# Optimization experiments

Hardware: AMD Instinct MI355X
Metric: run time of the kernel (lower is better)

Reference implementation:

```python
import jax, jax.numpy as jnp
import numpy as np

N, TI, ENC_DIM, DEC_DIM, ATT_DIM = 32, 2000, 512, 512, 512


def setup_inputs() -> dict:
    key = jax.random.key(0)
    ks = jax.random.split(key, 8)
    enc_pad = jax.random.normal(ks[0], (N, TI, ENC_DIM), dtype=jnp.float32)
    dec_prev = jax.random.normal(ks[1], (N, DEC_DIM), dtype=jnp.float32)
    ali_prev = jax.random.uniform(ks[2], (N, TI), dtype=jnp.float32)
    # lengths in [Ti//2, Ti], force one full-length row (module uses max(enc_len) as mask width)
    enc_len = jax.random.randint(ks[3], (N,), TI // 2, TI + 1)
    enc_len = enc_len.at[0].set(TI)
    # learned params (nn.Linear layout: W [out, in])
    s_e = 1.0 / np.sqrt(ENC_DIM)
    s_d = 1.0 / np.sqrt(DEC_DIM)
    s_a = 1.0 / np.sqrt(ATT_DIM)
    W_enc = jax.random.uniform(ks[4], (ATT_DIM, ENC_DIM), minval=-s_e, maxval=s_e, dtype=jnp.float32)
    b_enc = jax.random.uniform(ks[5], (ATT_DIM,), minval=-s_e, maxval=s_e, dtype=jnp.float32)
    W_dec = jax.random.uniform(ks[6], (ATT_DIM, DEC_DIM), minval=-s_d, maxval=s_d, dtype=jnp.float32)
    w_v = jax.random.uniform(ks[7], (ATT_DIM,), minval=-s_a, maxval=s_a, dtype=jnp.float32)
    return {"enc_pad": enc_pad, "enc_len": enc_len, "dec_prev": dec_prev,
            "ali_prev": ali_prev, "W_enc": W_enc, "b_enc": b_enc,
            "W_dec": W_dec, "w_v": w_v}


def reference(enc_pad, enc_len, dec_prev, ali_prev, W_enc, b_enc, W_dec, w_v):
    # enc_part: N x Ti x A  (enc_proj with bias)
    enc_part = jnp.einsum('ntd,ad->nta', enc_pad, W_enc) + b_enc
    # dec_part: N x A  (dec_proj, no bias)
    dec_part = jnp.einsum('nd,ad->na', dec_prev, W_dec)
    # additive score e = w^T tanh(enc_part + dec_part): N x Ti
    e = jnp.einsum('nta,a->nt', jnp.tanh(enc_part + dec_part[:, None, :]), w_v)
    # padding mask: positions >= enc_len are masked
    mask = jnp.arange(e.shape[1]) >= enc_len[:, None]  # N x Ti
    e = jnp.where(mask, -jnp.inf, e)
    ali = jax.nn.softmax(e, axis=1)  # N x Ti
    ctx = jnp.einsum('nt,ntd->nd', ali, enc_pad)  # N x D_enc
    return (ali, ctx)
```

## Files before the change

### kernel.cpp

```cpp
#include <hip/hip_runtime.h>
#include <stdint.h>


#define NB  32
#define TI  2000
#define ED  512
#define AD  512
#define M_TOT (NB * TI)
#define NSPLIT 20
#define TCHUNK (TI / NSPLIT)
#define MT  500
#define MT2 250
#define KT  8
#define TILE_BYTES  16384
#define TILE_HALVES 8192

using f16x8 = __attribute__((ext_vector_type(8))) _Float16;
using f32x4 = __attribute__((ext_vector_type(4))) float;

__device__ __forceinline__ int swz(int r, int c) { return (r * 128 + c) ^ ((r & 7) << 4); }

#define GLD16(g, l)                                                     \
    __builtin_amdgcn_global_load_lds(                                   \
        (const __attribute__((address_space(1))) void*)(g),             \
        (__attribute__((address_space(3))) void*)(l), 16, 0, 0)

__device__ __forceinline__ float fast_tanh(float s) {
    s = fminf(fmaxf(s, -15.f), 15.f);
    float t = __expf(2.f * s);
    return __fdividef(t - 1.f, t + 1.f);
}

__global__ void k_convert(const float* __restrict__ enc, const float* __restrict__ Wenc,
                          _Float16* __restrict__ X16, _Float16* __restrict__ W16,
                          const float* __restrict__ dec_prev, const float* __restrict__ W_dec,
                          const float* __restrict__ b_enc, float* __restrict__ db) {
    __shared__ float xd[ED];
    int bx = blockIdx.x;
    int tid = threadIdx.x;
    if (bx >= MT * KT + 32) {
        int n = bx - (MT * KT + 32);
        for (int k = tid; k < ED; k += 256) xd[k] = dec_prev[n * ED + k];
        __syncthreads();
        for (int a = tid; a < AD; a += 256) {
            const float* wr = W_dec + (size_t)a * ED;
            float s = 0.f;
#pragma unroll 8
            for (int k = 0; k < ED; k += 4) {
                float4 w = *(const float4*)(wr + k);
                s += xd[k] * w.x + xd[k + 1] * w.y + xd[k + 2] * w.z + xd[k + 3] * w.w;
            }
            db[n * AD + a] = s + b_enc[a];
        }
        return;
    }
    const float* src;
    char* dstb;
    if (bx < MT * KT) {
        int mt = bx >> 3, kt = bx & 7;
        src  = enc + (size_t)mt * 128 * ED + kt * 64;
        dstb = (char*)(X16 + (size_t)bx * TILE_HALVES);
    } else {
        int wt = bx - MT * KT;
        int at = wt >> 3, kt = wt & 7;
        src  = Wenc + (size_t)at * 128 * ED + kt * 64;
        dstb = (char*)(W16 + (size_t)wt * TILE_HALVES);
    }
#pragma unroll
    for (int i = 0; i < 4; ++i) {
        int o  = i * 4096 + tid * 16;
        int r  = o >> 7;
        int c2 = o & 127;
        const float* s = src + (size_t)r * ED + (c2 >> 1);
        float4 a = *(const float4*)s;
        float4 b = *(const float4*)(s + 4);
        f16x8 h;
        h[0] = (_Float16)a.x; h[1] = (_Float16)a.y; h[2] = (_Float16)a.z; h[3] = (_Float16)a.w;
        h[4] = (_Float16)b.x; h[5] = (_Float16)b.y; h[6] = (_Float16)b.z; h[7] = (_Float16)b.w;
        *(f16x8*)(dstb + swz(r, c2)) = h;
    }
}

__global__ void k_decdb(const float* __restrict__ dec_prev,
                        const float* __restrict__ W_dec,
                        const float* __restrict__ b_enc,
                        float* __restrict__ db) {
    int n = blockIdx.x;
    __shared__ float xd[ED];
    for (int k = threadIdx.x; k < ED; k += 256) xd[k] = dec_prev[n * ED + k];
    __syncthreads();
    for (int a = threadIdx.x; a < AD; a += 256) {
        const float* wr = W_dec + (size_t)a * ED;
        float s = 0.f;
#pragma unroll 8
        for (int k = 0; k < ED; k += 4) {
            float4 w = *(const float4*)(wr + k);
            s += xd[k] * w.x + xd[k + 1] * w.y + xd[k + 2] * w.z + xd[k + 3] * w.w;
        }
        db[n * AD + a] = s + b_enc[a];
    }
}

__device__ __forceinline__ void stage_tiles(const char* xb, const char* wb,
                                            char* dA, char* dB, int kt, int o) {
    const char* xs = xb + kt * TILE_BYTES + o;
    const char* ws = wb + kt * TILE_BYTES + o;
    GLD16(xs,                           dA + o);
    GLD16(xs + 8192,                    dA + o + 8192);
    GLD16(xs + KT * TILE_BYTES,         dA + o + 16384);
    GLD16(xs + KT * TILE_BYTES + 8192,  dA + o + 24576);
    GLD16(ws,                           dB + o);
    GLD16(ws + 8192,                    dB + o + 8192);
    GLD16(ws + KT * TILE_BYTES,         dB + o + 16384);
    GLD16(ws + KT * TILE_BYTES + 8192,  dB + o + 24576);
}

__launch_bounds__(512, 2)
__global__ void k_score256(const _Float16* __restrict__ X16, const _Float16* __restrict__ W16,
                           const float* __restrict__ db, const float* __restrict__ wv,
                           float* __restrict__ e_part) {
    __shared__ alignas(16) char As0[32768];
    __shared__ alignas(16) char As1[32768];
    __shared__ alignas(16) char Bs0[32768];
    __shared__ alignas(16) char Bs1[32768];

    int fid = blockIdx.x;
    int g = fid >> 4, r = fid & 15;
    int at2 = r >> 3;
    int mt2 = g * 8 + (r & 7);
    if (mt2 >= MT2) return;

    const int tid  = threadIdx.x;
    const int lane = tid & 63;
    const int w    = tid >> 6;
    const int wm   = w >> 2;
    const int wn   = w & 3;
    const int m0   = mt2 * 256;
    const int a0   = at2 * 256;

    const char* xb = (const char*)X16 + (size_t)(mt2 * 2 * KT) * TILE_BYTES;
    const char* wb = (const char*)W16 + (size_t)(at2 * 2 * KT) * TILE_BYTES;

    const int lr    = lane & 15;
    const int lk2   = (lane >> 4) * 16;
    const int wmoff = wm * 16384;
    const int wnoff = (wn >> 1) * 16384;
    const int wnrow = (wn & 1) * 64;
    const int o     = tid * 16;

    f32x4 acc[8][4];
#pragma unroll
    for (int rb = 0; rb < 8; ++rb)
#pragma unroll
        for (int cb = 0; cb < 4; ++cb) acc[rb][cb] = (f32x4){0.f, 0.f, 0.f, 0.f};

#define COMPUTE(sA, sB)                                                          \
    {                                                                            \
        _Pragma("unroll")                                                        \
        for (int kb = 0; kb < 2; ++kb) {                                         \
            f16x8 aF[8], bF[4];                                                  \
            _Pragma("unroll")                                                    \
            for (int rb = 0; rb < 8; ++rb)                                       \
                aF[rb] = *(const f16x8*)((sA) + wmoff + swz(rb * 16 + lr, kb * 64 + lk2)); \
            _Pragma("unroll")                                                    \
            for (int cb = 0; cb < 4; ++cb)                                       \
                bF[cb] = *(const f16x8*)((sB) + wnoff + swz(wnrow + cb * 16 + lr, kb * 64 + lk2)); \
            __builtin_amdgcn_s_setprio(1);                                       \
            _Pragma("unroll")                                                    \
            for (int rb = 0; rb < 8; ++rb)                                       \
                _Pragma("unroll")                                                \
                for (int cb = 0; cb < 4; ++cb)                                   \
                    acc[rb][cb] = __builtin_amdgcn_mfma_f32_16x16x32_f16(        \
                        aF[rb], bF[cb], acc[rb][cb], 0, 0, 0);                   \
            __builtin_amdgcn_s_setprio(0);                                       \
        }                                                                        \
    }

    stage_tiles(xb, wb, As0, Bs0, 0, o); __syncthreads();
    stage_tiles(xb, wb, As1, Bs1, 1, o); COMPUTE(As0, Bs0); __syncthreads();
    stage_tiles(xb, wb, As0, Bs0, 2, o); COMPUTE(As1, Bs1); __syncthreads();
    stage_tiles(xb, wb, As1, Bs1, 3, o); COMPUTE(As0, Bs0); __syncthreads();
    stage_tiles(xb, wb, As0, Bs0, 4, o); COMPUTE(As1, Bs1); __syncthreads();
    stage_tiles(xb, wb, As1, Bs1, 5, o); COMPUTE(As0, Bs0); __syncthreads();
    stage_tiles(xb, wb, As0, Bs0, 6, o); COMPUTE(As1, Bs1); __syncthreads();
    stage_tiles(xb, wb, As1, Bs1, 7, o); COMPUTE(As0, Bs0); __syncthreads();
    COMPUTE(As1, Bs1); __syncthreads();
#undef COMPUTE

    float* e_red = (float*)As0;
    const int lg = lane >> 4;
    float wvv[4];
#pragma unroll
    for (int cb = 0; cb < 4; ++cb) wvv[cb] = wv[a0 + wn * 64 + cb * 16 + lr];

#pragma unroll
    for (int rb = 0; rb < 8; ++rb) {
#pragma unroll
        for (int i = 0; i < 4; ++i) {
            int row_local = wm * 128 + rb * 16 + lg * 4 + i;
            int m = m0 + row_local;
            int n = m / TI;
            const float* dbp = db + (size_t)n * AD + a0 + wn * 64;
            float rs = 0.f;
#pragma unroll
            for (int cb = 0; cb < 4; ++cb) {
                float s = acc[rb][cb][i] + dbp[cb * 16 + lr];
                rs += fast_tanh(s) * wvv[cb];
            }
            rs += __shfl_xor(rs, 1);
            rs += __shfl_xor(rs, 2);
            rs += __shfl_xor(rs, 4);
            rs += __shfl_xor(rs, 8);
            if (lr == 0) e_red[wn * 256 + row_local] = rs;
        }
    }
    __syncthreads();
    if (tid < 256)
        e_part[(size_t)at2 * M_TOT + m0 + tid] =
            e_red[tid] + e_red[256 + tid] + e_red[512 + tid] + e_red[768 + tid];
}

__launch_bounds__(256, 2)
__global__ void k_score_fb(const float* __restrict__ X, const float* __restrict__ W,
                           const float* __restrict__ db, const float* __restrict__ wv,
                           float* __restrict__ e_part) {
    __shared__ alignas(16) _Float16 Xs[128][72];
    __shared__ alignas(16) _Float16 Ws[128][72];
    __shared__ float e_red[2][128];

    const int tid = threadIdx.x, lane = tid & 63, wid = tid >> 6;
    const int wr = wid >> 1, wc = wid & 1;
    const int m0 = blockIdx.x * 128, a0 = blockIdx.y * 128;

    f32x4 acc[4][4];
#pragma unroll
    for (int rb = 0; rb < 4; ++rb)
#pragma unroll
        for (int cb = 0; cb < 4; ++cb) acc[rb][cb] = (f32x4){0.f, 0.f, 0.f, 0.f};

    const int lr = lane & 15;
    const int lk = (lane >> 4) << 3;

    for (int kt = 0; kt < ED; kt += 64) {
#pragma unroll
        for (int i = 0; i < 4; ++i) {
            int idx = tid + i * 256, r = idx >> 3, c = (idx & 7) << 3;
            const float* gx = X + (size_t)(m0 + r) * ED + kt + c;
            float4 x0 = *(const float4*)gx, x1 = *(const float4*)(gx + 4);
            f16x8 hx;
            hx[0] = (_Float16)x0.x; hx[1] = (_Float16)x0.y; hx[2] = (_Float16)x0.z; hx[3] = (_Float16)x0.w;
            hx[4] = (_Float16)x1.x; hx[5] = (_Float16)x1.y; hx[6] = (_Float16)x1.z; hx[7] = (_Float16)x1.w;
            *(f16x8*)&Xs[r][c] = hx;
            const float* gw = W + (size_t)(a0 + r) * ED + kt + c;
            float4 w0 = *(const float4*)gw, w1 = *(const float4*)(gw + 4);
            f16x8 hw;
            hw[0] = (_Float16)w0.x; hw[1] = (_Float16)w0.y; hw[2] = (_Float16)w0.z; hw[3] = (_Float16)w0.w;
            hw[4] = (_Float16)w1.x; hw[5] = (_Float16)w1.y; hw[6] = (_Float16)w1.z; hw[7] = (_Float16)w1.w;
            *(f16x8*)&Ws[r][c] = hw;
        }
        __syncthreads();
#pragma unroll
        for (int kb = 0; kb < 64; kb += 32) {
            f16x8 aF[4], bF[4];
#pragma unroll
            for (int rb = 0; rb < 4; ++rb) aF[rb] = *(const f16x8*)&Xs[wr * 64 + rb * 16 + lr][kb + lk];
#pragma unroll
            for (int cb = 0; cb < 4; ++cb) bF[cb] = *(const f16x8*)&Ws[wc * 64 + cb * 16 + lr][kb + lk];
#pragma unroll
            for (int rb = 0; rb < 4; ++rb)
#pragma unroll
                for (int cb = 0; cb < 4; ++cb)
                    acc[rb][cb] = __builtin_amdgcn_mfma_f32_16x16x32_f16(aF[rb], bF[cb], acc[rb][cb], 0, 0, 0);
        }
        __syncthreads();
    }

    const int lg = lane >> 4;
    float wvv[4];
#pragma unroll
    for (int cb = 0; cb < 4; ++cb) wvv[cb] = wv[a0 + wc * 64 + cb * 16 + lr];
#pragma unroll
    for (int rb = 0; rb < 4; ++rb) {
#pragma unroll
        for (int i = 0; i < 4; ++i) {
            int row_local = wr * 64 + rb * 16 + lg * 4 + i;
            int m = m0 + row_local;
            int n = m / TI;
            const float* dbp = db + (size_t)n * AD + a0 + wc * 64;
            float rs = 0.f;
#pragma unroll
            for (int cb = 0; cb < 4; ++cb) {
                float s = acc[rb][cb][i] + dbp[cb * 16 + lr];
                rs += fast_tanh(s) * wvv[cb];
            }
            rs += __shfl_xor(rs, 1);
            rs += __shfl_xor(rs, 2);
            rs += __shfl_xor(rs, 4);
            rs += __shfl_xor(rs, 8);
            if (lr == 0) e_red[wc][row_local] = rs;
        }
    }
    __syncthreads();
    if (tid < 128)
        e_part[(size_t)blockIdx.y * M_TOT + m0 + tid] = e_red[0][tid] + e_red[1][tid];
}

__global__ void k_softmax(const float* __restrict__ e_part,
                          const int* __restrict__ enc_len,
                          float* __restrict__ ali, int nparts) {
    int n = blockIdx.x;
    int len = enc_len[n];
    __shared__ float se[TI];
    __shared__ float redm[4];
    __shared__ float reds[4];
    int tid = threadIdx.x;
    int lane = tid & 63, wid = tid >> 6;

    for (int t = tid; t < TI; t += 256) {
        float s = 0.f;
        for (int p = 0; p < nparts; ++p) s += e_part[(size_t)p * M_TOT + n * TI + t];
        se[t] = s;
    }
    __syncthreads();

    float mx = -1e30f;
    for (int t = tid; t < len; t += 256) mx = fmaxf(mx, se[t]);
#pragma unroll
    for (int o = 32; o >= 1; o >>= 1) mx = fmaxf(mx, __shfl_xor(mx, o));
    if (lane == 0) redm[wid] = mx;
    __syncthreads();
    mx = fmaxf(fmaxf(redm[0], redm[1]), fmaxf(redm[2], redm[3]));

    float sm = 0.f;
    for (int t = tid; t < len; t += 256) {
        float ex = __expf(se[t] - mx);
        se[t] = ex;
        sm += ex;
    }
#pragma unroll
    for (int o = 32; o >= 1; o >>= 1) sm += __shfl_xor(sm, o);
    if (lane == 0) reds[wid] = sm;
    __syncthreads();
    float inv = 1.f / (reds[0] + reds[1] + reds[2] + reds[3]);

    for (int t = tid; t < TI; t += 256)
        ali[n * TI + t] = (t < len) ? se[t] * inv : 0.f;
}

__global__ void k_ctxpart16(const _Float16* __restrict__ X16, const float* __restrict__ ali,
                            float* __restrict__ cpart) {
    int s = blockIdx.x, n = blockIdx.y;
    int tid = threadIdx.x;
    int sub = tid >> 6;
    int dc  = (tid & 63) * 8;
    int ktile = dc >> 6;
    int c2 = (dc & 63) * 2;
    float acc[8] = {0.f, 0.f, 0.f, 0.f, 0.f, 0.f, 0.f, 0.f};
    for (int t = s * TCHUNK + sub; t < (s + 1) * TCHUNK; t += 4) {
        int m = n * TI + t;
        int mt2 = m >> 7, r = m & 127;
        const char* p = (const char*)(X16 + (size_t)(mt2 * KT + ktile) * TILE_HALVES);
        f16x8 v = *(const f16x8*)(p + swz(r, c2));
        float a = ali[m];
#pragma unroll
        for (int j = 0; j < 8; ++j) acc[j] = fmaf(a, (float)v[j], acc[j]);
    }
    __shared__ float red[4][ED];
#pragma unroll
    for (int j = 0; j < 8; ++j) red[sub][dc + j] = acc[j];
    __syncthreads();
    if (sub == 0) {
#pragma unroll
        for (int j = 0; j < 8; ++j) {
            float sm = red[0][dc + j] + red[1][dc + j] + red[2][dc + j] + red[3][dc + j];
            cpart[((size_t)(n * NSPLIT + s)) * ED + dc + j] = sm;
        }
    }
}

__global__ void k_ctxpart(const float* __restrict__ enc,
                          const float* __restrict__ ali,
                          float* __restrict__ cpart) {
    int s = blockIdx.x;
    int n = blockIdx.y;
    int d0 = threadIdx.x * 2;
    const float* base = enc + ((size_t)n * TI + s * TCHUNK) * ED + d0;
    const float* ap = ali + n * TI + s * TCHUNK;
    float ax = 0.f, ay = 0.f;
#pragma unroll 4
    for (int t = 0; t < TCHUNK; ++t) {
        float a = ap[t];
        float2 v = *(const float2*)(base + (size_t)t * ED);
        ax = fmaf(a, v.x, ax);
        ay = fmaf(a, v.y, ay);
    }
    float2 r; r.x = ax; r.y = ay;
    *(float2*)&cpart[((size_t)(n * NSPLIT + s)) * ED + d0] = r;
}

__global__ void k_ctxred(const float* __restrict__ cpart, float* __restrict__ ctx) {
    int n = blockIdx.x;
    for (int d = threadIdx.x; d < ED; d += 256) {
        float sum = 0.f;
#pragma unroll
        for (int s = 0; s < NSPLIT; ++s) sum += cpart[((size_t)(n * NSPLIT + s)) * ED + d];
        ctx[(size_t)n * ED + d] = sum;
    }
}

extern "C" void kernel_launch(void* const* d_in, const int* in_sizes, int n_in,
                              void* d_out, int out_size, void* d_ws, size_t ws_size,
                              hipStream_t stream) {
    const float* enc_pad  = (const float*)d_in[0];
    const int*   enc_len  = (const int*)d_in[1];
    const float* dec_prev = (const float*)d_in[2];
    const float* W_enc    = (const float*)d_in[4];
    const float* b_enc    = (const float*)d_in[5];
    const float* W_dec    = (const float*)d_in[6];
    const float* w_v      = (const float*)d_in[7];

    float* out = (float*)d_out;
    float* ali = out;
    float* ctx = out + M_TOT;

    float* ws     = (float*)d_ws;
    float* db     = ws;
    float* e_part = ws + NB * AD;
    float* cpart  = e_part + 4 * M_TOT;
    size_t fp_floats = (size_t)NB * AD + 4 * M_TOT + (size_t)NB * NSPLIT * ED;
    _Float16* X16 = (_Float16*)((char*)d_ws + fp_floats * 4);
    _Float16* W16 = X16 + (size_t)MT * KT * TILE_HALVES;
    size_t need = fp_floats * 4 + ((size_t)MT * KT + 32) * TILE_BYTES;
    bool big = ws_size >= need;

    if (big) {
        hipLaunchKernelGGL(k_convert, dim3(MT * KT + 64), dim3(256), 0, stream,
                           enc_pad, W_enc, X16, W16, dec_prev, W_dec, b_enc, db);
        hipLaunchKernelGGL(k_score256, dim3(512), dim3(512), 0, stream,
                           X16, W16, db, w_v, e_part);
        hipLaunchKernelGGL(k_softmax, dim3(NB), dim3(256), 0, stream, e_part, enc_len, ali, 2);
        hipLaunchKernelGGL(k_ctxpart16, dim3(NSPLIT, NB), dim3(256), 0, stream, X16, ali, cpart);
    } else {
        hipLaunchKernelGGL(k_decdb, dim3(NB), dim3(256), 0, stream, dec_prev, W_dec, b_enc, db);
        hipLaunchKernelGGL(k_score_fb, dim3(MT, 4), dim3(256), 0, stream,
                           enc_pad, W_enc, db, w_v, e_part);
        hipLaunchKernelGGL(k_softmax, dim3(NB), dim3(256), 0, stream, e_part, enc_len, ali, 4);
        hipLaunchKernelGGL(k_ctxpart, dim3(NSPLIT, NB), dim3(256), 0, stream, enc_pad, ali, cpart);
    }
    hipLaunchKernelGGL(k_ctxred, dim3(NB), dim3(256), 0, stream, cpart, ctx);
}
```

Before: 138.9 us.

## Convert encoder fp32 to fp16 inside score GEMM instead of a separate pre-pass

Drops the pre-pass that converted the whole encoder tensor to a swizzled fp16 copy in workspace. The score GEMM now loads fp32 encoder rows into registers, converts them and writes swizzled fp16 into LDS. These register loads are issued before the MFMA compute of the current tile so they overlap it. Only W_enc is still pre-converted. The context reduction now reads fp32 encoder data with twice as many splits, which removes the fp16 scratch write and re-read but doubles that kernel's bytes read and raises register pressure in the GEMM.

```diff
diff --git a/kernel.cpp b/kernel.cpp
--- a/kernel.cpp
+++ b/kernel.cpp
@@ -7,9 +7,8 @@
 #define ED  512
 #define AD  512
 #define M_TOT (NB * TI)
-#define NSPLIT 20
+#define NSPLIT 40
 #define TCHUNK (TI / NSPLIT)
-#define MT  500
 #define MT2 250
 #define KT  8
 #define TILE_BYTES  16384
@@ -31,15 +30,21 @@
     return __fdividef(t - 1.f, t + 1.f);
 }
 
-__global__ void k_convert(const float* __restrict__ enc, const float* __restrict__ Wenc,
-                          _Float16* __restrict__ X16, _Float16* __restrict__ W16,
-                          const float* __restrict__ dec_prev, const float* __restrict__ W_dec,
-                          const float* __restrict__ b_enc, float* __restrict__ db) {
+__device__ __forceinline__ f16x8 cvt8(float4 a, float4 b) {
+    f16x8 h;
+    h[0] = (_Float16)a.x; h[1] = (_Float16)a.y; h[2] = (_Float16)a.z; h[3] = (_Float16)a.w;
+    h[4] = (_Float16)b.x; h[5] = (_Float16)b.y; h[6] = (_Float16)b.z; h[7] = (_Float16)b.w;
+    return h;
+}
+
+__global__ void k_wconvert(const float* __restrict__ Wenc, _Float16* __restrict__ W16,
+                           const float* __restrict__ dec_prev, const float* __restrict__ W_dec,
+                           const float* __restrict__ b_enc, float* __restrict__ db) {
     __shared__ float xd[ED];
     int bx = blockIdx.x;
     int tid = threadIdx.x;
-    if (bx >= MT * KT + 32) {
-        int n = bx - (MT * KT + 32);
+    if (bx >= 128) {
+        int n = bx - 128;
         for (int k = tid; k < ED; k += 256) xd[k] = dec_prev[n * ED + k];
         __syncthreads();
         for (int a = tid; a < AD; a += 256) {
@@ -54,69 +59,20 @@
         }
         return;
     }
-    const float* src;
-    char* dstb;
-    if (bx < MT * KT) {
-        int mt = bx >> 3, kt = bx & 7;
-        src  = enc + (size_t)mt * 128 * ED + kt * 64;
-        dstb = (char*)(X16 + (size_t)bx * TILE_HALVES);
-    } else {
-        int wt = bx - MT * KT;
-        int at = wt >> 3, kt = wt & 7;
-        src  = Wenc + (size_t)at * 128 * ED + kt * 64;
-        dstb = (char*)(W16 + (size_t)wt * TILE_HALVES);
-    }
-#pragma unroll
-    for (int i = 0; i < 4; ++i) {
-        int o  = i * 4096 + tid * 16;
-        int r  = o >> 7;
-        int c2 = o & 127;
-        const float* s = src + (size_t)r * ED + (c2 >> 1);
-        float4 a = *(const float4*)s;
-        float4 b = *(const float4*)(s + 4);
-        f16x8 h;
-        h[0] = (_Float16)a.x; h[1] = (_Float16)a.y; h[2] = (_Float16)a.z; h[3] = (_Float16)a.w;
-        h[4] = (_Float16)b.x; h[5] = (_Float16)b.y; h[6] = (_Float16)b.z; h[7] = (_Float16)b.w;
-        *(f16x8*)(dstb + swz(r, c2)) = h;
-    }
-}
-
-__global__ void k_decdb(const float* __restrict__ dec_prev,
-                        const float* __restrict__ W_dec,
-                        const float* __restrict__ b_enc,
-                        float* __restrict__ db) {
-    int n = blockIdx.x;
-    __shared__ float xd[ED];
-    for (int k = threadIdx.x; k < ED; k += 256) xd[k] = dec_prev[n * ED + k];
-    __syncthreads();
-    for (int a = threadIdx.x; a < AD; a += 256) {
-        const float* wr = W_dec + (size_t)a * ED;
-        float s = 0.f;
-#pragma unroll 8
-        for (int k = 0; k < ED; k += 4) {
-            float4 w = *(const float4*)(wr + k);
-            s += xd[k] * w.x + xd[k + 1] * w.y + xd[k + 2] * w.z + xd[k + 3] * w.w;
-        }
-        db[n * AD + a] = s + b_enc[a];
-    }
-}
-
-__device__ __forceinline__ void stage_tiles(const char* xb, const char* wb,
-                                            char* dA, char* dB, int kt, int o) {
-    const char* xs = xb + kt * TILE_BYTES + o;
-    const char* ws = wb + kt * TILE_BYTES + o;
-    GLD16(xs,                           dA + o);
-    GLD16(xs + 8192,                    dA + o + 8192);
-    GLD16(xs + KT * TILE_BYTES,         dA + o + 16384);
-    GLD16(xs + KT * TILE_BYTES + 8192,  dA + o + 24576);
-    GLD16(ws,                           dB + o);
-    GLD16(ws + 8192,                    dB + o + 8192);
-    GLD16(ws + KT * TILE_BYTES,         dB + o + 16384);
-    GLD16(ws + KT * TILE_BYTES + 8192,  dB + o + 24576);
+    int idx = bx * 4096 + tid * 16;
+    int wt  = idx >> 14;
+    int o   = idx & 16383;
+    int r   = o >> 7;
+    int c2  = o & 127;
+    int at  = wt >> 3, kt = wt & 7;
+    const float* s = Wenc + ((size_t)(at * 128 + r)) * ED + kt * 64 + (c2 >> 1);
+    float4 a = *(const float4*)s;
+    float4 b = *(const float4*)(s + 4);
+    *(f16x8*)((char*)W16 + (wt << 14) + swz(r, c2)) = cvt8(a, b);
 }
 
 __launch_bounds__(512, 2)
-__global__ void k_score256(const _Float16* __restrict__ X16, const _Float16* __restrict__ W16,
+__global__ void k_score256(const float* __restrict__ enc, const _Float16* __restrict__ W16,
                            const float* __restrict__ db, const float* __restrict__ wv,
                            float* __restrict__ e_part) {
     __shared__ alignas(16) char As0[32768];
@@ -138,7 +94,6 @@
     const int m0   = mt2 * 256;
     const int a0   = at2 * 256;
 
-    const char* xb = (const char*)X16 + (size_t)(mt2 * 2 * KT) * TILE_BYTES;
     const char* wb = (const char*)W16 + (size_t)(at2 * 2 * KT) * TILE_BYTES;
 
     const int lr    = lane & 15;
@@ -148,11 +103,51 @@
     const int wnrow = (wn & 1) * 64;
     const int o     = tid * 16;
 
+    const int arow  = tid >> 1;
+    const float* abase = enc + (size_t)(m0 + arow) * ED + (tid & 1) * 32;
+    char* const awbase = ((arow >> 7) ? (char*)0 : (char*)0);
+    const int arr   = arow & 127;
+    const int astrip = (arow >> 7) * 16384;
+    const int acb   = (tid & 1) * 64;
+
     f32x4 acc[8][4];
 #pragma unroll
     for (int rb = 0; rb < 8; ++rb)
 #pragma unroll
         for (int cb = 0; cb < 4; ++cb) acc[rb][cb] = (f32x4){0.f, 0.f, 0.f, 0.f};
+
+    float4 va0, va1, va2, va3, va4, va5, va6, va7;
+
+#define STAGE_A_LOAD(kt)                                        \
+    {                                                           \
+        const float* ap = abase + (kt) * 64;                    \
+        va0 = *(const float4*)(ap + 0);                         \
+        va1 = *(const float4*)(ap + 4);                         \
+        va2 = *(const float4*)(ap + 8);                         \
+        va3 = *(const float4*)(ap + 12);                        \
+        va4 = *(const float4*)(ap + 16);                        \
+        va5 = *(const float4*)(ap + 20);                        \
+        va6 = *(const float4*)(ap + 24);                        \
+        va7 = *(const float4*)(ap + 28);                        \
+    }
+
+#define STAGE_A_WRITE(dst)                                      \
+    {                                                           \
+        char* ab = (dst) + astrip;                              \
+        *(f16x8*)(ab + swz(arr, acb + 0))  = cvt8(va0, va1);    \
+        *(f16x8*)(ab + swz(arr, acb + 16)) = cvt8(va2, va3);    \
+        *(f16x8*)(ab + swz(arr, acb + 32)) = cvt8(va4, va5);    \
+        *(f16x8*)(ab + swz(arr, acb + 48)) = cvt8(va6, va7);    \
+    }
+
+#define STAGE_B(kt, dB)                                         \
+    {                                                           \
+        const char* ws_ = wb + (kt) * TILE_BYTES + o;           \
+        GLD16(ws_,                          (dB) + o);          \
+        GLD16(ws_ + 8192,                   (dB) + o + 8192);   \
+        GLD16(ws_ + KT * TILE_BYTES,        (dB) + o + 16384);  \
+        GLD16(ws_ + KT * TILE_BYTES + 8192, (dB) + o + 24576);  \
+    }
 
 #define COMPUTE(sA, sB)                                                          \
     {                                                                            \
@@ -176,16 +171,34 @@
         }                                                                        \
     }
 
-    stage_tiles(xb, wb, As0, Bs0, 0, o); __syncthreads();
-    stage_tiles(xb, wb, As1, Bs1, 1, o); COMPUTE(As0, Bs0); __syncthreads();
-    stage_tiles(xb, wb, As0, Bs0, 2, o); COMPUTE(As1, Bs1); __syncthreads();
-    stage_tiles(xb, wb, As1, Bs1, 3, o); COMPUTE(As0, Bs0); __syncthreads();
-    stage_tiles(xb, wb, As0, Bs0, 4, o); COMPUTE(As1, Bs1); __syncthreads();
-    stage_tiles(xb, wb, As1, Bs1, 5, o); COMPUTE(As0, Bs0); __syncthreads();
-    stage_tiles(xb, wb, As0, Bs0, 6, o); COMPUTE(As1, Bs1); __syncthreads();
-    stage_tiles(xb, wb, As1, Bs1, 7, o); COMPUTE(As0, Bs0); __syncthreads();
-    COMPUTE(As1, Bs1); __syncthreads();
+#define ITER(kt, Acur, Bcur, Anxt, Bnxt)                        \
+    STAGE_A_LOAD(kt + 1);                                       \
+    STAGE_B(kt + 1, Bnxt);                                      \
+    __builtin_amdgcn_sched_barrier(0);                          \
+    COMPUTE(Acur, Bcur);                                        \
+    __builtin_amdgcn_sched_barrier(0);                          \
+    STAGE_A_WRITE(Anxt);                                        \
+    __syncthreads();
+
+    STAGE_A_LOAD(0);
+    STAGE_B(0, Bs0);
+    STAGE_A_WRITE(As0);
+    __syncthreads();
+
+    ITER(0, As0, Bs0, As1, Bs1)
+    ITER(1, As1, Bs1, As0, Bs0)
+    ITER(2, As0, Bs0, As1, Bs1)
+    ITER(3, As1, Bs1, As0, Bs0)
+    ITER(4, As0, Bs0, As1, Bs1)
+    ITER(5, As1, Bs1, As0, Bs0)
+    ITER(6, As0, Bs0, As1, Bs1)
+    COMPUTE(As1, Bs1);
+    __syncthreads();
+#undef ITER
 #undef COMPUTE
+#undef STAGE_B
+#undef STAGE_A_WRITE
+#undef STAGE_A_LOAD
 
     float* e_red = (float*)As0;
     const int lg = lane >> 4;
@@ -220,6 +233,26 @@
             e_red[tid] + e_red[256 + tid] + e_red[512 + tid] + e_red[768 + tid];
 }
 
+__global__ void k_decdb(const float* __restrict__ dec_prev,
+                        const float* __restrict__ W_dec,
+                        const float* __restrict__ b_enc,
+                        float* __restrict__ db) {
+    int n = blockIdx.x;
+    __shared__ float xd[ED];
+    for (int k = threadIdx.x; k < ED; k += 256) xd[k] = dec_prev[n * ED + k];
+    __syncthreads();
+    for (int a = threadIdx.x; a < AD; a += 256) {
+        const float* wr = W_dec + (size_t)a * ED;
+        float s = 0.f;
+#pragma unroll 8
+        for (int k = 0; k < ED; k += 4) {
+            float4 w = *(const float4*)(wr + k);
+            s += xd[k] * w.x + xd[k + 1] * w.y + xd[k + 2] * w.z + xd[k + 3] * w.w;
+        }
+        db[n * AD + a] = s + b_enc[a];
+    }
+}
+
 __launch_bounds__(256, 2)
 __global__ void k_score_fb(const float* __restrict__ X, const float* __restrict__ W,
                            const float* __restrict__ db, const float* __restrict__ wv,
@@ -247,16 +280,10 @@
             int idx = tid + i * 256, r = idx >> 3, c = (idx & 7) << 3;
             const float* gx = X + (size_t)(m0 + r) * ED + kt + c;
             float4 x0 = *(const float4*)gx, x1 = *(const float4*)(gx + 4);
-            f16x8 hx;
-            hx[0] = (_Float16)x0.x; hx[1] = (_Float16)x0.y; hx[2] = (_Float16)x0.z; hx[3] = (_Float16)x0.w;
-            hx[4] = (_Float16)x1.x; hx[5] = (_Float16)x1.y; hx[6] = (_Float16)x1.z; hx[7] = (_Float16)x1.w;
-            *(f16x8*)&Xs[r][c] = hx;
+            *(f16x8*)&Xs[r][c] = cvt8(x0, x1);
             const float* gw = W + (size_t)(a0 + r) * ED + kt + c;
             float4 w0 = *(const float4*)gw, w1 = *(const float4*)(gw + 4);
-            f16x8 hw;
-            hw[0] = (_Float16)w0.x; hw[1] = (_Float16)w0.y; hw[2] = (_Float16)w0.z; hw[3] = (_Float16)w0.w;
-            hw[4] = (_Float16)w1.x; hw[5] = (_Float16)w1.y; hw[6] = (_Float16)w1.z; hw[7] = (_Float16)w1.w;
-            *(f16x8*)&Ws[r][c] = hw;
+            *(f16x8*)&Ws[r][c] = cvt8(w0, w1);
         }
         __syncthreads();
 #pragma unroll
@@ -347,37 +374,6 @@
         ali[n * TI + t] = (t < len) ? se[t] * inv : 0.f;
 }
 
-__global__ void k_ctxpart16(const _Float16* __restrict__ X16, const float* __restrict__ ali,
-                            float* __restrict__ cpart) {
-    int s = blockIdx.x, n = blockIdx.y;
-    int tid = threadIdx.x;
-    int sub = tid >> 6;
-    int dc  = (tid & 63) * 8;
-    int ktile = dc >> 6;
-    int c2 = (dc & 63) * 2;
-    float acc[8] = {0.f, 0.f, 0.f, 0.f, 0.f, 0.f, 0.f, 0.f};
-    for (int t = s * TCHUNK + sub; t < (s + 1) * TCHUNK; t += 4) {
-        int m = n * TI + t;
-        int mt2 = m >> 7, r = m & 127;
-        const char* p = (const char*)(X16 + (size_t)(mt2 * KT + ktile) * TILE_HALVES);
-        f16x8 v = *(const f16x8*)(p + swz(r, c2));
-        float a = ali[m];
-#pragma unroll
-        for (int j = 0; j < 8; ++j) acc[j] = fmaf(a, (float)v[j], acc[j]);
-    }
-    __shared__ float red[4][ED];
-#pragma unroll
-    for (int j = 0; j < 8; ++j) red[sub][dc + j] = acc[j];
-    __syncthreads();
-    if (sub == 0) {
-#pragma unroll
-        for (int j = 0; j < 8; ++j) {
-            float sm = red[0][dc + j] + red[1][dc + j] + red[2][dc + j] + red[3][dc + j];
-            cpart[((size_t)(n * NSPLIT + s)) * ED + dc + j] = sm;
-        }
-    }
-}
-
 __global__ void k_ctxpart(const float* __restrict__ enc,
                           const float* __restrict__ ali,
                           float* __restrict__ cpart) {
@@ -387,7 +383,7 @@
     const float* base = enc + ((size_t)n * TI + s * TCHUNK) * ED + d0;
     const float* ap = ali + n * TI + s * TCHUNK;
     float ax = 0.f, ay = 0.f;
-#pragma unroll 4
+#pragma unroll 5
     for (int t = 0; t < TCHUNK; ++t) {
         float a = ap[t];
         float2 v = *(const float2*)(base + (size_t)t * ED);
@@ -428,24 +424,22 @@
     float* e_part = ws + NB * AD;
     float* cpart  = e_part + 4 * M_TOT;
     size_t fp_floats = (size_t)NB * AD + 4 * M_TOT + (size_t)NB * NSPLIT * ED;
-    _Float16* X16 = (_Float16*)((char*)d_ws + fp_floats * 4);
-    _Float16* W16 = X16 + (size_t)MT * KT * TILE_HALVES;
-    size_t need = fp_floats * 4 + ((size_t)MT * KT + 32) * TILE_BYTES;
+    _Float16* W16 = (_Float16*)((char*)d_ws + fp_floats * 4);
+    size_t need = fp_floats * 4 + (size_t)32 * TILE_BYTES;
     bool big = ws_size >= need;
 
     if (big) {
-        hipLaunchKernelGGL(k_convert, dim3(MT * KT + 64), dim3(256), 0, stream,
-                           enc_pad, W_enc, X16, W16, dec_prev, W_dec, b_enc, db);
+        hipLaunchKernelGGL(k_wconvert, dim3(160), dim3(256), 0, stream,
+                           W_enc, W16, dec_prev, W_dec, b_enc, db);
         hipLaunchKernelGGL(k_score256, dim3(512), dim3(512), 0, stream,
-                           X16, W16, db, w_v, e_part);
+                           enc_pad, W16, db, w_v, e_part);
         hipLaunchKernelGGL(k_softmax, dim3(NB), dim3(256), 0, stream, e_part, enc_len, ali, 2);
-        hipLaunchKernelGGL(k_ctxpart16, dim3(NSPLIT, NB), dim3(256), 0, stream, X16, ali, cpart);
     } else {
         hipLaunchKernelGGL(k_decdb, dim3(NB), dim3(256), 0, stream, dec_prev, W_dec, b_enc, db);
-        hipLaunchKernelGGL(k_score_fb, dim3(MT, 4), dim3(256), 0, stream,
+        hipLaunchKernelGGL(k_score_fb, dim3(M_TOT / 128, 4), dim3(256), 0, stream,
                            enc_pad, W_enc, db, w_v, e_part);
         hipLaunchKernelGGL(k_softmax, dim3(NB), dim3(256), 0, stream, e_part, enc_len, ali, 4);
-        hipLaunchKernelGGL(k_ctxpart, dim3(NSPLIT, NB), dim3(256), 0, stream, enc_pad, ali, cpart);
-    }
+    }
+    hipLaunchKernelGGL(k_ctxpart, dim3(NSPLIT, NB), dim3(256), 0, stream, enc_pad, ali, cpart);
     hipLaunchKernelGGL(k_ctxred, dim3(NB), dim3(256), 0, stream, cpart, ctx);
 }
```

After: 166.4 us. +19.9%, slower.
